# Kernel optimization log

Hardware: AMD Instinct MI355X
Metric: run time of the kernel (lower is better)

Reference implementation:

```python
import jax, jax.numpy as jnp
import numpy as np
from jax import lax

B, C, H, W = 32, 1, 512, 512

def kernel_gauss_2d(m=3, sigma=3):
    x = np.arange(-m, m + 0.1)
    X, Y = np.meshgrid(x, x)
    g = np.exp(-(X ** 2 + Y ** 2) / (2 * sigma ** 2))
    g /= np.sum(g)
    return g.astype(np.float32)

KERNEL33 = (0.25 * np.array([[0., 1., 0.], [1., 0., 1.], [0., 1., 0.]], dtype=np.float32))
KERNEL_GAUSS = kernel_gauss_2d(m=3, sigma=3)  # 7x7


def _conv(x, w, pad):
    # NCHW conv, stride 1, symmetric padding
    return lax.conv_general_dilated(
        x, w, window_strides=(1, 1), padding=[(pad, pad), (pad, pad)],
        dimension_numbers=("NCHW", "OIHW", "NCHW"))


def _maxpool(x, k, pad):
    return lax.reduce_window(
        x, -jnp.inf, lax.max,
        window_dimensions=(1, 1, k, k), window_strides=(1, 1, 1, 1),
        padding=[(0, 0), (0, 0), (pad, pad), (pad, pad)])


def setup_inputs() -> dict:
    key = jax.random.key(0)
    ks = jax.random.split(key, 9)
    d = {"X": jax.random.normal(ks[0], (B, C, H, W), dtype=jnp.float32)}
    d["w0"] = jax.random.normal(ks[1], (2, 1, 1, 1), dtype=jnp.float32) * 0.5
    d["b0"] = jax.random.normal(ks[2], (2,), dtype=jnp.float32) * 0.1
    for i in range(1, 7):
        d[f"w{i}"] = jax.random.normal(ks[2 + i], (2, 1, 1, 1), dtype=jnp.float32) * 0.5
    return d


def reference(X, w0, b0, w1, w2, w3, w4, w5, w6):
    k33 = jnp.asarray(KERNEL33).reshape(1, 1, 3, 3)
    kg = jnp.asarray(KERNEL_GAUSS).reshape(1, 1, 7, 7)

    X1 = _conv(X, k33, pad=1)                 # fixed 3x3 blur
    X2 = _conv(X, kg, pad=3)                  # fixed 7x7 gaussian
    X3 = -_maxpool(-X, 3, pad=1)              # 3x3 min-pool
    X4 = -_maxpool(-X, 11, pad=5)             # 11x11 min-pool
    X5 = _maxpool(X, 3, pad=1)                # 3x3 max-pool
    X6 = _maxpool(X, 11, pad=5)               # 11x11 max-pool

    out = _conv(X, w0, 0) + b0.reshape(1, 2, 1, 1)
    out = out + _conv(X1, w1, 0) + _conv(X2, w2, 0) + _conv(X3, w3, 0)
    out = out + _conv(X4, w4, 0) + _conv(X5, w5, 0) + _conv(X6, w6, 0)
    return out
```

## Files before the change

### kernel.cpp

```cpp
#include <hip/hip_runtime.h>

#define IMG 512
#define TW 64
#define TH 16
#define GST 64

__device__ __forceinline__ float nan0(float v){ return v==v ? v : 0.0f; }
__device__ __forceinline__ float min3f(float a,float b,float c){ return fminf(fminf(a,b),c); }
__device__ __forceinline__ float max3f(float a,float b,float c){ return fmaxf(fmaxf(a,b),c); }
__device__ __forceinline__ unsigned pk2(float lo, float hi){
    return (__float_as_uint(hi) & 0xFFFF0000u) | (__float_as_uint(lo) >> 16);
}
__device__ __forceinline__ float up_lo(unsigned u){ return __uint_as_float(u << 16); }
__device__ __forceinline__ float up_hi(unsigned u){ return __uint_as_float(u & 0xFFFF0000u); }

__global__ __launch_bounds__(256)
void simplenet_fused(const float* __restrict__ X,
                     const float* __restrict__ w0, const float* __restrict__ b0,
                     const float* __restrict__ w1, const float* __restrict__ w2,
                     const float* __restrict__ w3, const float* __restrict__ w4,
                     const float* __restrict__ w5, const float* __restrict__ w6,
                     float* __restrict__ out)
{
    __shared__ float    GH [22*GST];
    __shared__ unsigned HNX[26*GST];

    const int tid = threadIdx.x;
    const int xo = tid & 63, ty = tid >> 6, y0 = ty*4;
    const int bx = blockIdx.x, by = blockIdx.y, bz = blockIdx.z;
    const int tx0 = bx*TW, ty0 = by*TH;
    const bool xe = (bx==0)||(bx==IMG/TW-1);
    const bool ye = (by==0)||(by==IMG/TH-1);
    const float* Xb = X + (size_t)bz*(IMG*IMG);
    const float qn = __builtin_nanf("");

    const float W0c0=w0[0], W0c1=w0[1], B0=b0[0], B1=b0[1];
    const float W1c0=w1[0], W1c1=w1[1], W2c0=w2[0], W2c1=w2[1];
    const float W3c0=w3[0], W3c1=w3[1], W4c0=w4[0], W4c1=w4[1];
    const float W5c0=w5[0], W5c1=w5[1], W6c0=w6[0], W6c1=w6[1];

    const float G0=0.10628875f, G1=0.14032194f, G2=0.16577342f, G3=0.17523179f;

    for (int t = tid; t < 26*16; t += 256) {
        const int r = t >> 4, g = t & 15;
        const int gy  = ty0 - 5 + r;
        const int gx0 = tx0 - 8 + 4*g;
        float x[20];
        const bool yv = !ye || ((unsigned)gy < IMG);
        if (yv) {
            if (!xe) {
#pragma unroll
                for (int j=0;j<5;++j) {
                    const float4 q = *(const float4*)(Xb + gy*IMG + gx0 + 4*j);
                    x[4*j]=q.x; x[4*j+1]=q.y; x[4*j+2]=q.z; x[4*j+3]=q.w;
                }
            } else {
                const float* row = Xb + gy*IMG;
#pragma unroll
                for (int j=0;j<5;++j) {
                    const int c0 = gx0 + 4*j;
                    if (c0 >= 0 && c0 + 3 < IMG) {
                        const float4 q = *(const float4*)(row + c0);
                        x[4*j]=q.x; x[4*j+1]=q.y; x[4*j+2]=q.z; x[4*j+3]=q.w;
                    } else {
#pragma unroll
                        for (int i=0;i<4;++i) {
                            const int gx = c0 + i;
                            const float v = row[min(max(gx,0),IMG-1)];
                            x[4*j+i] = ((unsigned)gx < IMG) ? v : qn;
                        }
                    }
                }
            }
        } else {
#pragma unroll
            for (int i=0;i<20;++i) x[i] = qn;
        }
        float mn[12], mx[12];
#pragma unroll
        for (int i=0;i<12;++i) {
            mn[i] = min3f(x[i+3],x[i+4],x[i+5]);
            mx[i] = max3f(x[i+3],x[i+4],x[i+5]);
        }
        unsigned hw[4];
#pragma unroll
        for (int k=0;k<4;++k) {
            const float hn = fminf(fminf(mn[k],mn[k+3]), fminf(mn[k+6],mn[k+8]));
            const float hx = fmaxf(fmaxf(mx[k],mx[k+3]), fmaxf(mx[k+6],mx[k+8]));
            hw[k] = pk2(hn, hx);
        }
        *(uint4*)&HNX[r*GST+4*g] = make_uint4(hw[0],hw[1],hw[2],hw[3]);
        if (r >= 2 && r < 24) {
            float zz[10];
#pragma unroll
            for (int j=0;j<10;++j) zz[j] = xe ? nan0(x[5+j]) : x[5+j];
            float gh4[4];
#pragma unroll
            for (int k=0;k<4;++k)
                gh4[k] = G0*(zz[k]+zz[k+6]) + G1*(zz[k+1]+zz[k+5]) + G2*(zz[k+2]+zz[k+4]) + G3*zz[k+3];
            *(float4*)&GH[(r-2)*GST+4*g] = make_float4(gh4[0],gh4[1],gh4[2],gh4[3]);
        }
    }

    float a0[4], a1[4];

    {
        const int gxc = tx0 + xo;
        float L[6], C[6], R[6];
        if (!xe && !ye) {
#pragma unroll
            for (int i=0;i<6;++i) {
                const float* row = Xb + (ty0+y0-1+i)*IMG + gxc;
                L[i]=row[-1]; C[i]=row[0]; R[i]=row[1];
            }
        } else {
#pragma unroll
            for (int i=0;i<6;++i) {
                const int gy = ty0+y0-1+i;
                const bool yv = (unsigned)gy < IMG;
                const float* row = Xb + (yv ? gy : 0)*IMG;
                float l = row[max(gxc-1,0)], c = row[gxc], r = row[min(gxc+1,IMG-1)];
                if (!yv) { l=qn; c=qn; r=qn; }
                if (gxc==0)     l=qn;
                if (gxc==IMG-1) r=qn;
                L[i]=l; C[i]=c; R[i]=r;
            }
        }
        float hm[6], hx6[6];
#pragma unroll
        for (int i=0;i<6;++i) { hm[i]=min3f(L[i],C[i],R[i]); hx6[i]=max3f(L[i],C[i],R[i]); }
        float Lz[6], Rz[6];
#pragma unroll
        for (int i=0;i<6;++i) { Lz[i] = xe ? nan0(L[i]) : L[i];
                                Rz[i] = xe ? nan0(R[i]) : R[i]; }
        const float Cz0 = ye ? nan0(C[0]) : C[0];
        const float Cz5 = ye ? nan0(C[5]) : C[5];
        const float up[4]={Cz0,C[1],C[2],C[3]};
        const float dn[4]={C[2],C[3],C[4],Cz5};
#pragma unroll
        for (int p=0;p<4;++p) {
            const float cr = 0.25f*(up[p] + dn[p] + Lz[p+1] + Rz[p+1]);
            a0[p] = B0 + W0c0*C[p+1] + W1c0*cr;
            a1[p] = B1 + W0c1*C[p+1] + W1c1*cr;
            const float mnv = min3f(hm[p],hm[p+1],hm[p+2]);
            const float mxv = max3f(hx6[p],hx6[p+1],hx6[p+2]);
            a0[p] += W3c0*mnv + W5c0*mxv;
            a1[p] += W3c1*mnv + W5c1*mxv;
        }
    }
    __syncthreads();

    {
        float wv[10];
        unsigned q[14];
#pragma unroll
        for (int i=0;i<10;++i) wv[i] = GH[(y0+i)*GST+xo];
#pragma unroll
        for (int i=0;i<14;++i) q[i]  = HNX[(y0+i)*GST+xo];
        if (ye) {
#pragma unroll
            for (int i=0;i<10;++i) wv[i] = nan0(wv[i]);
        }
#pragma unroll
        for (int p=0;p<4;++p) {
            const float s = G0*(wv[p]+wv[p+6]) + G1*(wv[p+1]+wv[p+5])
                          + G2*(wv[p+2]+wv[p+4]) + G3*wv[p+3];
            a0[p] += W2c0*s; a1[p] += W2c1*s;
        }
        float hn[14], hx[14];
#pragma unroll
        for (int i=0;i<14;++i) { hn[i]=up_lo(q[i]); hx[i]=up_hi(q[i]); }
        float an = hn[10], ax = hx[10];
#pragma unroll
        for (int i=9;i>=4;--i) { an=fminf(an,hn[i]); ax=fmaxf(ax,hx[i]); }
        const float Sn3=fminf(an,hn[3]),  Sx3=fmaxf(ax,hx[3]);
        const float Sn2=fminf(Sn3,hn[2]), Sx2=fmaxf(Sx3,hx[2]);
        const float Sn1=fminf(Sn2,hn[1]), Sx1=fmaxf(Sx2,hx[1]);
        const float Sn0=fminf(Sn1,hn[0]), Sx0=fmaxf(Sx1,hx[0]);
        const float pn1=hn[11],            px1=hx[11];
        const float pn2=fminf(pn1,hn[12]), px2=fmaxf(px1,hx[12]);
        const float pn3=fminf(pn2,hn[13]), px3=fmaxf(px2,hx[13]);
        const float on[4]={Sn0, fminf(Sn1,pn1), fminf(Sn2,pn2), fminf(Sn3,pn3)};
        const float ox[4]={Sx0, fmaxf(Sx1,px1), fmaxf(Sx2,px2), fmaxf(Sx3,px3)};
#pragma unroll
        for (int p=0;p<4;++p) {
            a0[p]+=W4c0*on[p]+W6c0*ox[p];
            a1[p]+=W4c1*on[p]+W6c1*ox[p];
        }
    }

    float* o0p = out + ((size_t)bz*2 + 0)*(IMG*IMG) + (size_t)(ty0+y0)*IMG + tx0 + xo;
    float* o1p = o0p + (IMG*IMG);
#pragma unroll
    for (int p=0;p<4;++p) {
        o0p[(size_t)p*IMG] = a0[p];
        o1p[(size_t)p*IMG] = a1[p];
    }
}

extern "C" void kernel_launch(void* const* d_in, const int* in_sizes, int n_in,
                              void* d_out, int out_size, void* d_ws, size_t ws_size,
                              hipStream_t stream) {
    const float* X  = (const float*)d_in[0];
    const float* w0 = (const float*)d_in[1];
    const float* b0 = (const float*)d_in[2];
    const float* w1 = (const float*)d_in[3];
    const float* w2 = (const float*)d_in[4];
    const float* w3 = (const float*)d_in[5];
    const float* w4 = (const float*)d_in[6];
    const float* w5 = (const float*)d_in[7];
    const float* w6 = (const float*)d_in[8];
    float* out = (float*)d_out;

    dim3 grid(IMG/TW, IMG/TH, 32);
    simplenet_fused<<<grid, 256, 0, stream>>>(X, w0, b0, w1, w2, w3, w4, w5, w6, out);
}
```

Before: 45.50 us.

## Double tile height, pack min/max-pool partials as fp16 pairs with packed min

Tile height goes from 16 to 32 rows with 512-thread blocks, which cuts the halo overhead of the 11-row pooling and 7-row Gaussian stages. The horizontal min/max partials are now stored as packed fp16 (min, negated max) pairs, so the vertical reduction runs as one packed min instead of two scalar bf16-style unpack chains. Edge handling is simplified to per-row and per-column bounds checks, with fp16 max values used as padding. The risks are fp16 precision and range for pool values (clipping above 65504, coarser rounding), more shared memory per block, and fewer resident blocks.

```diff
diff --git a/kernel.cpp b/kernel.cpp
--- a/kernel.cpp
+++ b/kernel.cpp
@@ -2,19 +2,19 @@
 
 #define IMG 512
 #define TW 64
-#define TH 16
+#define TH 32
+#define GROWS 38
+#define PROWS 42
 #define GST 64
+
+typedef __fp16 h2v __attribute__((ext_vector_type(2)));
+union UH { unsigned u; h2v h; };
 
 __device__ __forceinline__ float nan0(float v){ return v==v ? v : 0.0f; }
 __device__ __forceinline__ float min3f(float a,float b,float c){ return fminf(fminf(a,b),c); }
 __device__ __forceinline__ float max3f(float a,float b,float c){ return fmaxf(fmaxf(a,b),c); }
-__device__ __forceinline__ unsigned pk2(float lo, float hi){
-    return (__float_as_uint(hi) & 0xFFFF0000u) | (__float_as_uint(lo) >> 16);
-}
-__device__ __forceinline__ float up_lo(unsigned u){ return __uint_as_float(u << 16); }
-__device__ __forceinline__ float up_hi(unsigned u){ return __uint_as_float(u & 0xFFFF0000u); }
-
-__global__ __launch_bounds__(256)
+
+__global__ __launch_bounds__(512)
 void simplenet_fused(const float* __restrict__ X,
                      const float* __restrict__ w0, const float* __restrict__ b0,
                      const float* __restrict__ w1, const float* __restrict__ w2,
@@ -22,8 +22,8 @@
                      const float* __restrict__ w5, const float* __restrict__ w6,
                      float* __restrict__ out)
 {
-    __shared__ float    GH [22*GST];
-    __shared__ unsigned HNX[26*GST];
+    __shared__ float    GH [GROWS*GST];
+    __shared__ unsigned HNX[PROWS*GST];
 
     const int tid = threadIdx.x;
     const int xo = tid & 63, ty = tid >> 6, y0 = ty*4;
@@ -41,40 +41,33 @@
 
     const float G0=0.10628875f, G1=0.14032194f, G2=0.16577342f, G3=0.17523179f;
 
-    for (int t = tid; t < 26*16; t += 256) {
+    for (int t = tid; t < PROWS*16; t += 512) {
         const int r = t >> 4, g = t & 15;
         const int gy  = ty0 - 5 + r;
         const int gx0 = tx0 - 8 + 4*g;
+        const int wb  = r*GST + 4*g;
+        if ((unsigned)gy >= IMG) {
+            *(uint4*)&HNX[wb] = make_uint4(0x7BFF7BFFu,0x7BFF7BFFu,0x7BFF7BFFu,0x7BFF7BFFu);
+            if (r >= 2 && r < 40)
+                *(float4*)&GH[(r-2)*GST+4*g] = make_float4(qn,qn,qn,qn);
+            continue;
+        }
         float x[20];
-        const bool yv = !ye || ((unsigned)gy < IMG);
-        if (yv) {
-            if (!xe) {
-#pragma unroll
-                for (int j=0;j<5;++j) {
-                    const float4 q = *(const float4*)(Xb + gy*IMG + gx0 + 4*j);
-                    x[4*j]=q.x; x[4*j+1]=q.y; x[4*j+2]=q.z; x[4*j+3]=q.w;
-                }
-            } else {
-                const float* row = Xb + gy*IMG;
-#pragma unroll
-                for (int j=0;j<5;++j) {
-                    const int c0 = gx0 + 4*j;
-                    if (c0 >= 0 && c0 + 3 < IMG) {
-                        const float4 q = *(const float4*)(row + c0);
-                        x[4*j]=q.x; x[4*j+1]=q.y; x[4*j+2]=q.z; x[4*j+3]=q.w;
-                    } else {
-#pragma unroll
-                        for (int i=0;i<4;++i) {
-                            const int gx = c0 + i;
-                            const float v = row[min(max(gx,0),IMG-1)];
-                            x[4*j+i] = ((unsigned)gx < IMG) ? v : qn;
-                        }
-                    }
-                }
+        const bool xs = (unsigned)gx0 > (unsigned)(IMG-20);
+        if (!xs) {
+#pragma unroll
+            for (int j=0;j<5;++j) {
+                const float4 q = *(const float4*)(Xb + gy*IMG + gx0 + 4*j);
+                x[4*j]=q.x; x[4*j+1]=q.y; x[4*j+2]=q.z; x[4*j+3]=q.w;
             }
         } else {
-#pragma unroll
-            for (int i=0;i<20;++i) x[i] = qn;
+            const float* row = Xb + gy*IMG;
+#pragma unroll
+            for (int i=0;i<20;++i) {
+                const int gx = gx0 + i;
+                const float v = row[min(max(gx,0),IMG-1)];
+                x[i] = ((unsigned)gx < IMG) ? v : qn;
+            }
         }
         float mn[12], mx[12];
 #pragma unroll
@@ -87,13 +80,14 @@
         for (int k=0;k<4;++k) {
             const float hn = fminf(fminf(mn[k],mn[k+3]), fminf(mn[k+6],mn[k+8]));
             const float hx = fmaxf(fmaxf(mx[k],mx[k+3]), fmaxf(mx[k+6],mx[k+8]));
-            hw[k] = pk2(hn, hx);
-        }
-        *(uint4*)&HNX[r*GST+4*g] = make_uint4(hw[0],hw[1],hw[2],hw[3]);
-        if (r >= 2 && r < 24) {
+            UH c; c.h = __builtin_amdgcn_cvt_pkrtz(hn, -hx);
+            hw[k] = c.u;
+        }
+        *(uint4*)&HNX[wb] = make_uint4(hw[0],hw[1],hw[2],hw[3]);
+        if (r >= 2 && r < 40) {
             float zz[10];
 #pragma unroll
-            for (int j=0;j<10;++j) zz[j] = xe ? nan0(x[5+j]) : x[5+j];
+            for (int j=0;j<10;++j) zz[j] = xs ? nan0(x[5+j]) : x[5+j];
             float gh4[4];
 #pragma unroll
             for (int k=0;k<4;++k)
@@ -152,11 +146,11 @@
 
     {
         float wv[10];
-        unsigned q[14];
+        h2v q[14];
 #pragma unroll
         for (int i=0;i<10;++i) wv[i] = GH[(y0+i)*GST+xo];
 #pragma unroll
-        for (int i=0;i<14;++i) q[i]  = HNX[(y0+i)*GST+xo];
+        for (int i=0;i<14;++i) { UH uu; uu.u = HNX[(y0+i)*GST+xo]; q[i] = uu.h; }
         if (ye) {
 #pragma unroll
             for (int i=0;i<10;++i) wv[i] = nan0(wv[i]);
@@ -167,25 +161,26 @@
                           + G2*(wv[p+2]+wv[p+4]) + G3*wv[p+3];
             a0[p] += W2c0*s; a1[p] += W2c1*s;
         }
-        float hn[14], hx[14];
-#pragma unroll
-        for (int i=0;i<14;++i) { hn[i]=up_lo(q[i]); hx[i]=up_hi(q[i]); }
-        float an = hn[10], ax = hx[10];
-#pragma unroll
-        for (int i=9;i>=4;--i) { an=fminf(an,hn[i]); ax=fmaxf(ax,hx[i]); }
-        const float Sn3=fminf(an,hn[3]),  Sx3=fmaxf(ax,hx[3]);
-        const float Sn2=fminf(Sn3,hn[2]), Sx2=fmaxf(Sx3,hx[2]);
-        const float Sn1=fminf(Sn2,hn[1]), Sx1=fmaxf(Sx2,hx[1]);
-        const float Sn0=fminf(Sn1,hn[0]), Sx0=fmaxf(Sx1,hx[0]);
-        const float pn1=hn[11],            px1=hx[11];
-        const float pn2=fminf(pn1,hn[12]), px2=fmaxf(px1,hx[12]);
-        const float pn3=fminf(pn2,hn[13]), px3=fmaxf(px2,hx[13]);
-        const float on[4]={Sn0, fminf(Sn1,pn1), fminf(Sn2,pn2), fminf(Sn3,pn3)};
-        const float ox[4]={Sx0, fmaxf(Sx1,px1), fmaxf(Sx2,px2), fmaxf(Sx3,px3)};
+        h2v s = q[10];
+#pragma unroll
+        for (int i=9;i>=4;--i) s = __builtin_elementwise_min(s, q[i]);
+        const h2v S3 = __builtin_elementwise_min(s,  q[3]);
+        const h2v S2 = __builtin_elementwise_min(S3, q[2]);
+        const h2v S1 = __builtin_elementwise_min(S2, q[1]);
+        const h2v S0 = __builtin_elementwise_min(S1, q[0]);
+        const h2v p1 = q[11];
+        const h2v p2 = __builtin_elementwise_min(p1, q[12]);
+        const h2v p3 = __builtin_elementwise_min(p2, q[13]);
+        const h2v o0 = S0;
+        const h2v o1 = __builtin_elementwise_min(S1, p1);
+        const h2v o2 = __builtin_elementwise_min(S2, p2);
+        const h2v o3 = __builtin_elementwise_min(S3, p3);
+        const float on[4] = {(float)o0[0], (float)o1[0], (float)o2[0], (float)o3[0]};
+        const float ox[4] = {-(float)o0[1], -(float)o1[1], -(float)o2[1], -(float)o3[1]};
 #pragma unroll
         for (int p=0;p<4;++p) {
-            a0[p]+=W4c0*on[p]+W6c0*ox[p];
-            a1[p]+=W4c1*on[p]+W6c1*ox[p];
+            a0[p] += W4c0*on[p] + W6c0*ox[p];
+            a1[p] += W4c1*on[p] + W6c1*ox[p];
         }
     }
 
@@ -213,5 +208,5 @@
     float* out = (float*)d_out;
 
     dim3 grid(IMG/TW, IMG/TH, 32);
-    simplenet_fused<<<grid, 256, 0, stream>>>(X, w0, b0, w1, w2, w3, w4, w5, w6, out);
+    simplenet_fused<<<grid, 512, 0, stream>>>(X, w0, b0, w1, w2, w3, w4, w5, w6, out);
 }
```

Measured after the change: 39.08 us. -14.1%, faster.
